# Optimization experiments

Measured on AMD Instinct MI355X. Metric: run time of the kernel, lower is better.

## Reference

```python
import jax, jax.numpy as jnp
import numpy as np

STRIDE_S, STRIDE_L = 8, 28


def _masked_mean(d, m):
    # d: [L,B,N] float, m: [L,B,N] bool -> mean over masked N, count
    c = m.sum(-1)
    mean = (d * m).sum(-1) / jnp.maximum(c, 1).astype(d.dtype)
    return mean, c


def _scale_stats(sel, idx, kernel, valid_flat):
    # sel: [L,B,N,C], idx: [L,B,N] int, kernel: [L,B,C,1], valid_flat: [B,HW] bool
    B = valid_flat.shape[0]
    # column mask: drop all-zero token columns (mask over batch+channel dims)
    col_valid = (jnp.abs(sel).sum(axis=(1, 3)) != 0)  # [L,N]
    # membership of each selected token index in the valid GT set.
    # isin(idx_token, idx_gt & idx_token) == valid[idx_token] elementwise.
    member = valid_flat[jnp.arange(B)[:, None], idx]  # [L,B,N] bool
    pos = member & col_valid[:, None, :]
    neg = (~member) & col_valid[:, None, :]
    # per-token L2 distance from anchor kernel
    anchor = kernel[..., 0]  # [L,B,C]
    diff = anchor[:, :, None, :] - sel  # [L,B,N,C]
    d = jnp.sqrt((diff * diff).sum(-1))  # [L,B,N]
    ap, pc = _masked_mean(d, pos)
    an, nc = _masked_mean(d, neg)
    # SoftMarginLoss(an - ap, y=1) = log(1 + exp(-(an - ap))) = softplus(ap - an)
    loss = jax.nn.softplus(ap - an)  # [L,B]
    active = (pc > 0) & (nc > 0)  # skip conditions of the torch loop
    return loss, active


def setup_inputs() -> dict:
    key = jax.random.key(0)
    ks = jax.random.split(key, 8)
    L, B, Ns, Nl, C, H, W = 4, 8, 1200, 128, 768, 448, 448
    return {
        "sel_tokens_s": jax.random.normal(ks[0], (L, B, Ns, C), jnp.float32),
        "idx_tokens_s": jax.random.randint(ks[1], (L, B, Ns), 0, (H // STRIDE_S) * (W // STRIDE_S), jnp.int64 if jax.config.jax_enable_x64 else jnp.int32).astype(jnp.int32),
        "sel_tokens_l": jax.random.normal(ks[2], (L, B, Nl, C), jnp.float32),
        "idx_tokens_l": jax.random.randint(ks[3], (L, B, Nl), 0, (H // STRIDE_L) * (W // STRIDE_L)).astype(jnp.int32),
        "kernel_s": jax.random.normal(ks[4], (L, B, C, 1), jnp.float32),
        "kernel_l": jax.random.normal(ks[5], (L, B, C, 1), jnp.float32),
        "f_k": jax.random.normal(ks[6], (B, 1, H, W), jnp.float32),
    }


def reference(sel_tokens_s, idx_tokens_s, sel_tokens_l, idx_tokens_l, kernel_s, kernel_l, f_k):
    B = f_k.shape[0]
    # nearest-neighbour downsample by 1/8 and 1/28 == strided slice (H,W divisible)
    valid_s = (f_k[:, :, ::STRIDE_S, ::STRIDE_S].sum(axis=1) > 0).reshape(B, -1)
    valid_l = (f_k[:, :, ::STRIDE_L, ::STRIDE_L].sum(axis=1) > 0).reshape(B, -1)
    loss_s, act_s = _scale_stats(sel_tokens_s, idx_tokens_s, kernel_s, valid_s)
    loss_l, act_l = _scale_stats(sel_tokens_l, idx_tokens_l, kernel_l, valid_l)
    # torch `continue` on the s-scale skip also skips the l-scale term
    act_l = act_l & act_s
    total = jnp.where(act_s, loss_s, 0.0).sum() + jnp.where(act_l, loss_l, 0.0).sum()
    times = act_s.sum() + act_l.sum()
    return jnp.where(times > 0, total / jnp.maximum(times, 1).astype(total.dtype), 0.0)
```

## Files before the change

### kernel.cpp

```cpp
#include <hip/hip_runtime.h>
#include <math.h>

constexpr int L_  = 4;
constexpr int B_  = 8;
constexpr int NS  = 1200;
constexpr int NL  = 128;
constexpr int C_  = 768;
constexpr int H_  = 448;
constexpr int W_  = 448;
constexpr int NVS = (H_ / 8)  * (W_ / 8);
constexpr int NVL = (H_ / 28) * (W_ / 28);
constexpr int ROWS_S = L_ * B_ * NS;
constexpr int ROWS_L = L_ * B_ * NL;
constexpr int ROWS   = ROWS_S + ROWS_L;

__global__ __launch_bounds__(256)
void k_valid(const float* __restrict__ f_k,
             unsigned char* __restrict__ valid_s,
             unsigned char* __restrict__ valid_l) {
    int i = blockIdx.x * 256 + threadIdx.x;
    if (i < B_ * NVS) {
        int b = i / NVS, p = i - b * NVS;
        int r = p / 56, c = p - r * 56;
        valid_s[i] = (f_k[b * H_ * W_ + r * 8 * W_ + c * 8] > 0.f) ? 1 : 0;
    } else {
        int j = i - B_ * NVS;
        if (j < B_ * NVL) {
            int b = j / NVL, p = j - b * NVL;
            int r = p / 16, c = p - r * 16;
            valid_l[j] = (f_k[b * H_ * W_ + r * 28 * W_ + c * 28] > 0.f) ? 1 : 0;
        }
    }
}

__global__ __launch_bounds__(256)
void k_dist(const float* __restrict__ sel_s, const float* __restrict__ sel_l,
            const float* __restrict__ ker_s, const float* __restrict__ ker_l,
            float* __restrict__ d_s, float* __restrict__ d_l,
            unsigned char* __restrict__ nz_s, unsigned char* __restrict__ nz_l) {
    const int lane = threadIdx.x & 63;
    const int wid  = threadIdx.x >> 6;
    long long row = (long long)blockIdx.x * 4 + wid;
    if (row >= ROWS) return;

    const float* sel; const float* ker; float* dout; unsigned char* nzout;
    long long r; int N;
    if (row < ROWS_S) { r = row;           N = NS; sel = sel_s; ker = ker_s; dout = d_s; nzout = nz_s; }
    else              { r = row - ROWS_S;  N = NL; sel = sel_l; ker = ker_l; dout = d_l; nzout = nz_l; }

    const int lb = (int)(r / N);
    const float4* __restrict__ srow = (const float4*)(sel + r * (long long)C_);
    const float4* __restrict__ arow = (const float4*)(ker + (long long)lb * C_);

    float acc = 0.f;
    int nz = 0;
#pragma unroll
    for (int j = 0; j < 3; ++j) {
        float4 s4 = srow[j * 64 + lane];
        float4 a4 = arow[j * 64 + lane];
        float dx = a4.x - s4.x, dy = a4.y - s4.y;
        float dz = a4.z - s4.z, dw = a4.w - s4.w;
        acc += dx * dx + dy * dy + dz * dz + dw * dw;
        nz |= (s4.x != 0.f) || (s4.y != 0.f) || (s4.z != 0.f) || (s4.w != 0.f);
    }
#pragma unroll
    for (int off = 32; off >= 1; off >>= 1) acc += __shfl_xor(acc, off, 64);
    int wnz = __any(nz);
    if (lane == 0) {
        dout[r]  = sqrtf(acc);
        nzout[r] = (unsigned char)(wnz ? 1 : 0);
    }
}

__global__ __launch_bounds__(256)
void k_colvalid(const unsigned char* __restrict__ nz_s,
                const unsigned char* __restrict__ nz_l,
                unsigned char* __restrict__ cv_s,
                unsigned char* __restrict__ cv_l) {
    int i = blockIdx.x * 256 + threadIdx.x;
    if (i < L_ * NS) {
        int l = i / NS, n = i - l * NS;
        int v = 0;
        for (int b = 0; b < B_; ++b) v |= nz_s[(l * B_ + b) * NS + n];
        cv_s[i] = (unsigned char)v;
    } else {
        int j = i - L_ * NS;
        if (j < L_ * NL) {
            int l = j / NL, n = j - l * NL;
            int v = 0;
            for (int b = 0; b < B_; ++b) v |= nz_l[(l * B_ + b) * NL + n];
            cv_l[j] = (unsigned char)v;
        }
    }
}

__global__ __launch_bounds__(256)
void k_stats(const float* __restrict__ d_s, const float* __restrict__ d_l,
             const int* __restrict__ idx_s, const int* __restrict__ idx_l,
             const unsigned char* __restrict__ valid_s,
             const unsigned char* __restrict__ valid_l,
             const unsigned char* __restrict__ cv_s,
             const unsigned char* __restrict__ cv_l,
             float* __restrict__ loss, int* __restrict__ act) {
    const int blk = blockIdx.x;
    const bool large = blk >= 32;
    const int lb = blk & 31;
    const int l = lb / B_, b = lb - l * B_;
    const int N  = large ? NL : NS;
    const int Nv = large ? NVL : NVS;
    const float* d           = large ? d_l : d_s;
    const int* idx           = large ? idx_l : idx_s;
    const unsigned char* val = large ? valid_l : valid_s;
    const unsigned char* cv  = large ? cv_l : cv_s;

    float sp = 0.f, sn = 0.f;
    int cp = 0, cn = 0;
    const long long rowbase = (long long)lb * N;
    for (int n = threadIdx.x; n < N; n += 256) {
        float dv   = d[rowbase + n];
        int member = val[b * Nv + idx[rowbase + n]];
        int colv   = cv[l * N + n];
        int pos = member & colv;
        int neg = (member ^ 1) & colv;
        sp += pos ? dv : 0.f;
        sn += neg ? dv : 0.f;
        cp += pos;
        cn += neg;
    }
#pragma unroll
    for (int off = 32; off >= 1; off >>= 1) {
        sp += __shfl_xor(sp, off, 64);
        sn += __shfl_xor(sn, off, 64);
        cp += __shfl_xor(cp, off, 64);
        cn += __shfl_xor(cn, off, 64);
    }
    __shared__ float ssp[4], ssn[4];
    __shared__ int   scp[4], scn[4];
    const int wid = threadIdx.x >> 6, lane = threadIdx.x & 63;
    if (lane == 0) { ssp[wid] = sp; ssn[wid] = sn; scp[wid] = cp; scn[wid] = cn; }
    __syncthreads();
    if (threadIdx.x == 0) {
        float SP = 0.f, SN = 0.f; int CP = 0, CN = 0;
        for (int w = 0; w < 4; ++w) { SP += ssp[w]; SN += ssn[w]; CP += scp[w]; CN += scn[w]; }
        float ap = SP / (float)(CP > 0 ? CP : 1);
        float an = SN / (float)(CN > 0 ? CN : 1);
        float x  = ap - an;
        loss[blk] = fmaxf(x, 0.f) + log1pf(expf(-fabsf(x)));
        act[blk]  = (CP > 0 && CN > 0) ? 1 : 0;
    }
}

__global__ __launch_bounds__(64)
void k_final(const float* __restrict__ loss, const int* __restrict__ act,
             float* __restrict__ out) {
    int i = threadIdx.x;
    float total = 0.f;
    int times = 0;
    if (i < 32) {
        int as = act[i];
        int al = act[32 + i] & as;
        total = (as ? loss[i] : 0.f) + (al ? loss[32 + i] : 0.f);
        times = as + al;
    }
#pragma unroll
    for (int off = 32; off >= 1; off >>= 1) {
        total += __shfl_xor(total, off, 64);
        times += __shfl_xor(times, off, 64);
    }
    if (i == 0) out[0] = (times > 0) ? (total / (float)times) : 0.f;
}

extern "C" void kernel_launch(void* const* d_in, const int* in_sizes, int n_in,
                              void* d_out, int out_size, void* d_ws, size_t ws_size,
                              hipStream_t stream) {
    const float* sel_s = (const float*)d_in[0];
    const int*   idx_s = (const int*)  d_in[1];
    const float* sel_l = (const float*)d_in[2];
    const int*   idx_l = (const int*)  d_in[3];
    const float* ker_s = (const float*)d_in[4];
    const float* ker_l = (const float*)d_in[5];
    const float* f_k   = (const float*)d_in[6];
    float* out = (float*)d_out;

    char* base = (char*)d_ws;
    size_t o = 0;
    auto alloc = [&](size_t sz) -> char* {
        char* p = base + o;
        o += (sz + 255) & ~(size_t)255;
        return p;
    };
    unsigned char* valid_s = (unsigned char*)alloc(B_ * NVS);
    unsigned char* valid_l = (unsigned char*)alloc(B_ * NVL);
    unsigned char* nz_s    = (unsigned char*)alloc(ROWS_S);
    unsigned char* nz_l    = (unsigned char*)alloc(ROWS_L);
    unsigned char* cv_s    = (unsigned char*)alloc(L_ * NS);
    unsigned char* cv_l    = (unsigned char*)alloc(L_ * NL);
    float* d_s  = (float*)alloc(ROWS_S * sizeof(float));
    float* d_l  = (float*)alloc(ROWS_L * sizeof(float));
    float* loss = (float*)alloc(64 * sizeof(float));
    int*   act  = (int*)alloc(64 * sizeof(int));

    k_valid<<<(B_ * NVS + B_ * NVL + 255) / 256, 256, 0, stream>>>(f_k, valid_s, valid_l);
    k_dist<<<ROWS / 4, 256, 0, stream>>>(sel_s, sel_l, ker_s, ker_l, d_s, d_l, nz_s, nz_l);
    k_colvalid<<<(L_ * NS + L_ * NL + 255) / 256, 256, 0, stream>>>(nz_s, nz_l, cv_s, cv_l);
    k_stats<<<64, 256, 0, stream>>>(d_s, d_l, idx_s, idx_l, valid_s, valid_l, cv_s, cv_l, loss, act);
    k_final<<<1, 64, 0, stream>>>(loss, act, out);
}
```

Before: 199.9 us.

## Fuse column-valid and final reduction into stats kernel; batch rows per wave in dist

The column-validity pass is folded into the stats kernel by computing it into shared memory per (l,b) block. The final reduction is done by the last-arriving block through an atomic counter, which is reset in the valid kernel. The stats kernel now handles both scales per block. The distance kernel assigns four rows per wave, loads the anchor once per wave and issues all row loads before computing, which raises memory-level parallelism. Together this removes two kernel launches, at the cost of each stats block redundantly reading the nz flags across the batch.

```diff
diff --git a/kernel.cpp b/kernel.cpp
--- a/kernel.cpp
+++ b/kernel.cpp
@@ -8,17 +8,21 @@
 constexpr int C_  = 768;
 constexpr int H_  = 448;
 constexpr int W_  = 448;
-constexpr int NVS = (H_ / 8)  * (W_ / 8);
-constexpr int NVL = (H_ / 28) * (W_ / 28);
+constexpr int NVS = 3136;
+constexpr int NVL = 256;
 constexpr int ROWS_S = L_ * B_ * NS;
 constexpr int ROWS_L = L_ * B_ * NL;
-constexpr int ROWS   = ROWS_S + ROWS_L;
+constexpr int RPB    = 16;
+constexpr int BLKS_S = ROWS_S / RPB;
+constexpr int BLKS_L = ROWS_L / RPB;
 
 __global__ __launch_bounds__(256)
 void k_valid(const float* __restrict__ f_k,
              unsigned char* __restrict__ valid_s,
-             unsigned char* __restrict__ valid_l) {
+             unsigned char* __restrict__ valid_l,
+             int* __restrict__ counter) {
     int i = blockIdx.x * 256 + threadIdx.x;
+    if (i == 0) *counter = 0;
     if (i < B_ * NVS) {
         int b = i / NVS, p = i - b * NVS;
         int r = p / 56, c = p - r * 56;
@@ -40,56 +44,53 @@
             unsigned char* __restrict__ nz_s, unsigned char* __restrict__ nz_l) {
     const int lane = threadIdx.x & 63;
     const int wid  = threadIdx.x >> 6;
-    long long row = (long long)blockIdx.x * 4 + wid;
-    if (row >= ROWS) return;
+    const int blk  = blockIdx.x;
 
     const float* sel; const float* ker; float* dout; unsigned char* nzout;
-    long long r; int N;
-    if (row < ROWS_S) { r = row;           N = NS; sel = sel_s; ker = ker_s; dout = d_s; nzout = nz_s; }
-    else              { r = row - ROWS_S;  N = NL; sel = sel_l; ker = ker_l; dout = d_l; nzout = nz_l; }
-
-    const int lb = (int)(r / N);
-    const float4* __restrict__ srow = (const float4*)(sel + r * (long long)C_);
-    const float4* __restrict__ arow = (const float4*)(ker + (long long)lb * C_);
-
-    float acc = 0.f;
-    int nz = 0;
-#pragma unroll
-    for (int j = 0; j < 3; ++j) {
-        float4 s4 = srow[j * 64 + lane];
-        float4 a4 = arow[j * 64 + lane];
-        float dx = a4.x - s4.x, dy = a4.y - s4.y;
-        float dz = a4.z - s4.z, dw = a4.w - s4.w;
-        acc += dx * dx + dy * dy + dz * dz + dw * dw;
-        nz |= (s4.x != 0.f) || (s4.y != 0.f) || (s4.z != 0.f) || (s4.w != 0.f);
-    }
-#pragma unroll
-    for (int off = 32; off >= 1; off >>= 1) acc += __shfl_xor(acc, off, 64);
-    int wnz = __any(nz);
-    if (lane == 0) {
-        dout[r]  = sqrtf(acc);
-        nzout[r] = (unsigned char)(wnz ? 1 : 0);
-    }
-}
-
-__global__ __launch_bounds__(256)
-void k_colvalid(const unsigned char* __restrict__ nz_s,
-                const unsigned char* __restrict__ nz_l,
-                unsigned char* __restrict__ cv_s,
-                unsigned char* __restrict__ cv_l) {
-    int i = blockIdx.x * 256 + threadIdx.x;
-    if (i < L_ * NS) {
-        int l = i / NS, n = i - l * NS;
-        int v = 0;
-        for (int b = 0; b < B_; ++b) v |= nz_s[(l * B_ + b) * NS + n];
-        cv_s[i] = (unsigned char)v;
-    } else {
-        int j = i - L_ * NS;
-        if (j < L_ * NL) {
-            int l = j / NL, n = j - l * NL;
-            int v = 0;
-            for (int b = 0; b < B_; ++b) v |= nz_l[(l * B_ + b) * NL + n];
-            cv_l[j] = (unsigned char)v;
+    int base, N;
+    if (blk < BLKS_S) { base = blk * RPB;            N = NS; sel = sel_s; ker = ker_s; dout = d_s; nzout = nz_s; }
+    else              { base = (blk - BLKS_S) * RPB; N = NL; sel = sel_l; ker = ker_l; dout = d_l; nzout = nz_l; }
+    const int lb = base / N;
+
+    const float4* __restrict__ arow = (const float4*)(ker + lb * C_);
+    float4 a0 = arow[lane], a1 = arow[64 + lane], a2 = arow[128 + lane];
+
+    const int r0 = base + wid * 4;
+    float4 s[4][3];
+#pragma unroll
+    for (int k = 0; k < 4; ++k) {
+        const float4* __restrict__ srow = (const float4*)(sel + (r0 + k) * C_);
+        s[k][0] = srow[lane];
+        s[k][1] = srow[64 + lane];
+        s[k][2] = srow[128 + lane];
+    }
+#pragma unroll
+    for (int k = 0; k < 4; ++k) {
+        float acc = 0.f; int nz = 0;
+        {
+            float4 sv = s[k][0];
+            float dx = a0.x - sv.x, dy = a0.y - sv.y, dz = a0.z - sv.z, dw = a0.w - sv.w;
+            acc += dx*dx + dy*dy + dz*dz + dw*dw;
+            nz |= (sv.x != 0.f) || (sv.y != 0.f) || (sv.z != 0.f) || (sv.w != 0.f);
+        }
+        {
+            float4 sv = s[k][1];
+            float dx = a1.x - sv.x, dy = a1.y - sv.y, dz = a1.z - sv.z, dw = a1.w - sv.w;
+            acc += dx*dx + dy*dy + dz*dz + dw*dw;
+            nz |= (sv.x != 0.f) || (sv.y != 0.f) || (sv.z != 0.f) || (sv.w != 0.f);
+        }
+        {
+            float4 sv = s[k][2];
+            float dx = a2.x - sv.x, dy = a2.y - sv.y, dz = a2.z - sv.z, dw = a2.w - sv.w;
+            acc += dx*dx + dy*dy + dz*dz + dw*dw;
+            nz |= (sv.x != 0.f) || (sv.y != 0.f) || (sv.z != 0.f) || (sv.w != 0.f);
+        }
+#pragma unroll
+        for (int off = 32; off >= 1; off >>= 1) acc += __shfl_xor(acc, off, 64);
+        int wnz = __any(nz);
+        if (lane == 0) {
+            dout[r0 + k]  = sqrtf(acc);
+            nzout[r0 + k] = (unsigned char)(wnz ? 1 : 0);
         }
     }
 }
@@ -99,75 +100,110 @@
              const int* __restrict__ idx_s, const int* __restrict__ idx_l,
              const unsigned char* __restrict__ valid_s,
              const unsigned char* __restrict__ valid_l,
-             const unsigned char* __restrict__ cv_s,
-             const unsigned char* __restrict__ cv_l,
-             float* __restrict__ loss, int* __restrict__ act) {
+             const unsigned char* __restrict__ nz_s,
+             const unsigned char* __restrict__ nz_l,
+             float* __restrict__ res,
+             int* __restrict__ counter,
+             float* __restrict__ out) {
     const int blk = blockIdx.x;
-    const bool large = blk >= 32;
-    const int lb = blk & 31;
-    const int l = lb / B_, b = lb - l * B_;
-    const int N  = large ? NL : NS;
-    const int Nv = large ? NVL : NVS;
-    const float* d           = large ? d_l : d_s;
-    const int* idx           = large ? idx_l : idx_s;
-    const unsigned char* val = large ? valid_l : valid_s;
-    const unsigned char* cv  = large ? cv_l : cv_s;
-
-    float sp = 0.f, sn = 0.f;
-    int cp = 0, cn = 0;
-    const long long rowbase = (long long)lb * N;
-    for (int n = threadIdx.x; n < N; n += 256) {
-        float dv   = d[rowbase + n];
-        int member = val[b * Nv + idx[rowbase + n]];
-        int colv   = cv[l * N + n];
-        int pos = member & colv;
-        int neg = (member ^ 1) & colv;
-        sp += pos ? dv : 0.f;
-        sn += neg ? dv : 0.f;
-        cp += pos;
-        cn += neg;
+    const int l = blk >> 3, b = blk & 7;
+    const int tid = threadIdx.x;
+
+    __shared__ unsigned char cvs[NS];
+    __shared__ unsigned char cvl[NL];
+    for (int n = tid; n < NS; n += 256) {
+        int v = 0;
+        for (int bb = 0; bb < B_; ++bb) v |= nz_s[(l * B_ + bb) * NS + n];
+        cvs[n] = (unsigned char)v;
+    }
+    for (int n = tid; n < NL; n += 256) {
+        int v = 0;
+        for (int bb = 0; bb < B_; ++bb) v |= nz_l[(l * B_ + bb) * NL + n];
+        cvl[n] = (unsigned char)v;
+    }
+    __syncthreads();
+
+    float sp[2] = {0.f, 0.f}, sn[2] = {0.f, 0.f};
+    int   cp[2] = {0, 0},     cn[2] = {0, 0};
+#pragma unroll
+    for (int sc = 0; sc < 2; ++sc) {
+        const int N  = sc ? NL : NS;
+        const int Nv = sc ? NVL : NVS;
+        const float* d           = sc ? d_l : d_s;
+        const int* idx           = sc ? idx_l : idx_s;
+        const unsigned char* val = sc ? valid_l : valid_s;
+        const unsigned char* cv  = sc ? cvl : cvs;
+        const int rb = blk * N;
+        for (int n = tid; n < N; n += 256) {
+            float dv   = d[rb + n];
+            int member = val[b * Nv + idx[rb + n]];
+            int colv   = cv[n];
+            int pos = member & colv;
+            int neg = (member ^ 1) & colv;
+            sp[sc] += pos ? dv : 0.f;
+            sn[sc] += neg ? dv : 0.f;
+            cp[sc] += pos;
+            cn[sc] += neg;
+        }
     }
 #pragma unroll
     for (int off = 32; off >= 1; off >>= 1) {
-        sp += __shfl_xor(sp, off, 64);
-        sn += __shfl_xor(sn, off, 64);
-        cp += __shfl_xor(cp, off, 64);
-        cn += __shfl_xor(cn, off, 64);
-    }
-    __shared__ float ssp[4], ssn[4];
-    __shared__ int   scp[4], scn[4];
-    const int wid = threadIdx.x >> 6, lane = threadIdx.x & 63;
-    if (lane == 0) { ssp[wid] = sp; ssn[wid] = sn; scp[wid] = cp; scn[wid] = cn; }
+#pragma unroll
+        for (int sc = 0; sc < 2; ++sc) {
+            sp[sc] += __shfl_xor(sp[sc], off, 64);
+            sn[sc] += __shfl_xor(sn[sc], off, 64);
+            cp[sc] += __shfl_xor(cp[sc], off, 64);
+            cn[sc] += __shfl_xor(cn[sc], off, 64);
+        }
+    }
+    __shared__ float wsp[2][4], wsn[2][4];
+    __shared__ int   wcp[2][4], wcn[2][4];
+    __shared__ int   islast;
+    const int wid = tid >> 6, lane = tid & 63;
+    if (lane == 0) {
+#pragma unroll
+        for (int sc = 0; sc < 2; ++sc) {
+            wsp[sc][wid] = sp[sc]; wsn[sc][wid] = sn[sc];
+            wcp[sc][wid] = cp[sc]; wcn[sc][wid] = cn[sc];
+        }
+    }
+    if (tid == 0) islast = 0;
     __syncthreads();
-    if (threadIdx.x == 0) {
-        float SP = 0.f, SN = 0.f; int CP = 0, CN = 0;
-        for (int w = 0; w < 4; ++w) { SP += ssp[w]; SN += ssn[w]; CP += scp[w]; CN += scn[w]; }
-        float ap = SP / (float)(CP > 0 ? CP : 1);
-        float an = SN / (float)(CN > 0 ? CN : 1);
-        float x  = ap - an;
-        loss[blk] = fmaxf(x, 0.f) + log1pf(expf(-fabsf(x)));
-        act[blk]  = (CP > 0 && CN > 0) ? 1 : 0;
-    }
-}
-
-__global__ __launch_bounds__(64)
-void k_final(const float* __restrict__ loss, const int* __restrict__ act,
-             float* __restrict__ out) {
-    int i = threadIdx.x;
-    float total = 0.f;
-    int times = 0;
-    if (i < 32) {
-        int as = act[i];
-        int al = act[32 + i] & as;
-        total = (as ? loss[i] : 0.f) + (al ? loss[32 + i] : 0.f);
-        times = as + al;
-    }
-#pragma unroll
-    for (int off = 32; off >= 1; off >>= 1) {
-        total += __shfl_xor(total, off, 64);
-        times += __shfl_xor(times, off, 64);
-    }
-    if (i == 0) out[0] = (times > 0) ? (total / (float)times) : 0.f;
+
+    if (tid == 0) {
+        float lossv[2]; int actv[2];
+#pragma unroll
+        for (int sc = 0; sc < 2; ++sc) {
+            float SP = 0.f, SN = 0.f; int CP = 0, CN = 0;
+            for (int w = 0; w < 4; ++w) { SP += wsp[sc][w]; SN += wsn[sc][w]; CP += wcp[sc][w]; CN += wcn[sc][w]; }
+            float ap = SP / (float)(CP > 0 ? CP : 1);
+            float an = SN / (float)(CN > 0 ? CN : 1);
+            float x  = ap - an;
+            lossv[sc] = fmaxf(x, 0.f) + log1pf(expf(-fabsf(x)));
+            actv[sc]  = (CP > 0 && CN > 0) ? 1 : 0;
+        }
+        actv[1] &= actv[0];
+        float contrib = (actv[0] ? lossv[0] : 0.f) + (actv[1] ? lossv[1] : 0.f);
+        float times   = (float)(actv[0] + actv[1]);
+        __hip_atomic_store(&res[2 * blk],     contrib, __ATOMIC_RELAXED, __HIP_MEMORY_SCOPE_AGENT);
+        __hip_atomic_store(&res[2 * blk + 1], times,   __ATOMIC_RELAXED, __HIP_MEMORY_SCOPE_AGENT);
+        int old = __hip_atomic_fetch_add(counter, 1, __ATOMIC_ACQ_REL, __HIP_MEMORY_SCOPE_AGENT);
+        islast = (old == 31) ? 1 : 0;
+    }
+    __syncthreads();
+    if (islast && wid == 0) {
+        float total = 0.f, times = 0.f;
+        if (lane < 32) {
+            total = __hip_atomic_load(&res[2 * lane],     __ATOMIC_RELAXED, __HIP_MEMORY_SCOPE_AGENT);
+            times = __hip_atomic_load(&res[2 * lane + 1], __ATOMIC_RELAXED, __HIP_MEMORY_SCOPE_AGENT);
+        }
+#pragma unroll
+        for (int off = 32; off >= 1; off >>= 1) {
+            total += __shfl_xor(total, off, 64);
+            times += __shfl_xor(times, off, 64);
+        }
+        if (lane == 0) out[0] = (times > 0.f) ? (total / times) : 0.f;
+    }
 }
 
 extern "C" void kernel_launch(void* const* d_in, const int* in_sizes, int n_in,
@@ -193,16 +229,13 @@
     unsigned char* valid_l = (unsigned char*)alloc(B_ * NVL);
     unsigned char* nz_s    = (unsigned char*)alloc(ROWS_S);
     unsigned char* nz_l    = (unsigned char*)alloc(ROWS_L);
-    unsigned char* cv_s    = (unsigned char*)alloc(L_ * NS);
-    unsigned char* cv_l    = (unsigned char*)alloc(L_ * NL);
-    float* d_s  = (float*)alloc(ROWS_S * sizeof(float));
-    float* d_l  = (float*)alloc(ROWS_L * sizeof(float));
-    float* loss = (float*)alloc(64 * sizeof(float));
-    int*   act  = (int*)alloc(64 * sizeof(int));
-
-    k_valid<<<(B_ * NVS + B_ * NVL + 255) / 256, 256, 0, stream>>>(f_k, valid_s, valid_l);
-    k_dist<<<ROWS / 4, 256, 0, stream>>>(sel_s, sel_l, ker_s, ker_l, d_s, d_l, nz_s, nz_l);
-    k_colvalid<<<(L_ * NS + L_ * NL + 255) / 256, 256, 0, stream>>>(nz_s, nz_l, cv_s, cv_l);
-    k_stats<<<64, 256, 0, stream>>>(d_s, d_l, idx_s, idx_l, valid_s, valid_l, cv_s, cv_l, loss, act);
-    k_final<<<1, 64, 0, stream>>>(loss, act, out);
-}
+    float* d_s   = (float*)alloc(ROWS_S * sizeof(float));
+    float* d_l   = (float*)alloc(ROWS_L * sizeof(float));
+    float* res   = (float*)alloc(64 * sizeof(float));
+    int*   cnt   = (int*)alloc(sizeof(int));
+
+    k_valid<<<(B_ * NVS + B_ * NVL + 255) / 256, 256, 0, stream>>>(f_k, valid_s, valid_l, cnt);
+    k_dist<<<BLKS_S + BLKS_L, 256, 0, stream>>>(sel_s, sel_l, ker_s, ker_l, d_s, d_l, nz_s, nz_l);
+    k_stats<<<32, 256, 0, stream>>>(d_s, d_l, idx_s, idx_l, valid_s, valid_l,
+                                    nz_s, nz_l, res, cnt, out);
+}
```

Measured after the change: 202.7 us. About the same (+1.4%).
